# Kernel tuning notes

Hardware: AMD Instinct MI355X
Metric: run time of the kernel (lower is better)

Reference implementation:

```python
import jax, jax.numpy as jnp
import numpy as np

H = 81  # number_of_cells
EPS = 1e-5

def setup_inputs() -> dict:
    key = jax.random.key(0)
    ks = jax.random.split(key, 16)
    B, T, F = 512, 1024, 128
    s_ih = 1.0 / np.sqrt(H)
    inp = {
        'x':     jax.random.normal(ks[0], (B, 1, T, F), dtype=jnp.float32),
        'W_ih':  jax.random.uniform(ks[1], (3 * H, F), jnp.float32, -s_ih, s_ih),
        'W_hh':  jax.random.uniform(ks[2], (3 * H, H), jnp.float32, -s_ih, s_ih),
        'b_ih':  jax.random.uniform(ks[3], (3 * H,), jnp.float32, -s_ih, s_ih),
        'b_hh':  jax.random.uniform(ks[4], (3 * H,), jnp.float32, -s_ih, s_ih),
        'fc_w':  jax.random.uniform(ks[5], (8, H), jnp.float32, -s_ih, s_ih),
        'fc_b':  jax.random.uniform(ks[6], (8,), jnp.float32, -s_ih, s_ih),
        'g1':    jnp.ones((8,), jnp.float32),
        'beta1': jnp.zeros((8,), jnp.float32),
        'fc1_w': jax.random.uniform(ks[7], (4, 8), jnp.float32, -np.sqrt(1/8), np.sqrt(1/8)),
        'fc1_b': jax.random.uniform(ks[8], (4,), jnp.float32, -np.sqrt(1/8), np.sqrt(1/8)),
        'g2':    jnp.ones((4,), jnp.float32),
        'beta2': jnp.zeros((4,), jnp.float32),
        'fc2_w': jax.random.uniform(ks[9], (1, 4), jnp.float32, -0.5, 0.5),
        'fc2_b': jax.random.uniform(ks[10], (1,), jnp.float32, -0.5, 0.5),
    }
    return inp

def _batchnorm(x, g, b):
    mu = jnp.mean(x, axis=0)
    var = jnp.var(x, axis=0)  # biased, as torch uses for normalization
    return (x - mu) * jax.lax.rsqrt(var + EPS) * g + b

def _gru_last_hidden(x, W_ih, W_hh, b_ih, b_hh):
    # x: [B, T, F]; PyTorch gate order: r, z, n
    B = x.shape[0]
    xg = jnp.einsum('btf,gf->tbg', x, W_ih) + b_ih  # [T, B, 3H]
    h0 = jnp.zeros((B, H), x.dtype)

    def step(h, xg_t):
        hg = h @ W_hh.T + b_hh
        xr, xz, xn = jnp.split(xg_t, 3, axis=-1)
        hr, hz, hn = jnp.split(hg, 3, axis=-1)
        r = jax.nn.sigmoid(xr + hr)
        z = jax.nn.sigmoid(xz + hz)
        n = jnp.tanh(xn + r * hn)
        h_new = (1.0 - z) * n + z * h
        return h_new, None

    h_last, _ = jax.lax.scan(step, h0, xg)
    return h_last  # [B, H]

def reference(x, W_ih, W_hh, b_ih, b_hh, fc_w, fc_b, g1, beta1, fc1_w, fc1_b, g2, beta2, fc2_w, fc2_b):
    B = x.shape[0]
    xs = x.reshape(B, x.shape[2], x.shape[3])  # view(B, T, F)
    h = _gru_last_hidden(xs, W_ih, W_hh, b_ih, b_hh)
    out = h @ fc_w.T + fc_b            # GRU0.fc on last timestep -> [B, 8]
    out = jax.nn.silu(out)
    out = _batchnorm(out, g1, beta1)
    out = jax.nn.silu(out @ fc1_w.T + fc1_b)
    out = _batchnorm(out, g2, beta2)
    out = out @ fc2_w.T + fc2_b        # [B, 1]
    return out
```

## Files before the change

kernel.cpp:

```cpp
#include <hip/hip_runtime.h>

#define B_  512
#define T_  1024
#define F_  128
#define H_  81
#define G3  243
#define GPX 244

typedef unsigned short u16;
typedef __attribute__((ext_vector_type(8))) short bf16x8;
typedef __attribute__((ext_vector_type(4))) float f32x4;
typedef __attribute__((ext_vector_type(2))) float f32x2;

__device__ __forceinline__ float bf2f(u16 u) {
    union { unsigned int i; float f; } v; v.i = ((unsigned int)u) << 16; return v.f;
}
__device__ __forceinline__ u16 f2bf(float f) {
    union { float f; unsigned int i; } v; v.f = f;
    unsigned int i = v.i;
    return (u16)((i + 0x7fffu + ((i >> 16) & 1u)) >> 16);
}
__device__ __forceinline__ float sigmoidf_(float x) { return 1.f / (1.f + __expf(-x)); }
__device__ __forceinline__ float tanhf_(float x) {
    float e = __expf(2.f * x);
    return 1.f - 2.f / (e + 1.f);
}
__device__ __forceinline__ void barrier_nodrain() {
    asm volatile("s_waitcnt lgkmcnt(0)\n\ts_barrier" ::: "memory");
}

__global__ void wsplit_kernel(const float* __restrict__ W,
                              u16* __restrict__ hi, u16* __restrict__ lo)
{
    const int i = blockIdx.x * 256 + threadIdx.x;
    if (i < G3 * F_) {
        const float v = W[i];
        const u16 h = f2bf(v);
        hi[i] = h;
        lo[i] = f2bf(v - bf2f(h));
    }
}

__global__ __launch_bounds__(256, 2) void xg_gemm(const float* __restrict__ x,
                                                  const u16* __restrict__ Whi,
                                                  const u16* __restrict__ Wlo,
                                                  const float* __restrict__ b_ih,
                                                  float* __restrict__ xg)
{
    __shared__ __align__(16) u16 ws_hi[G3][64];
    __shared__ __align__(16) u16 ws_lo[G3][64];

    const int tid  = threadIdx.x;
    const int wave = tid >> 6, lane = tid & 63;
    const int l15  = lane & 15, q = lane >> 4;
    const int b    = blockIdx.x & 511;
    const int t0   = (blockIdx.x >> 9) << 7;

    f32x4 acc[2][16];
#pragma unroll
    for (int mt = 0; mt < 2; ++mt)
#pragma unroll
        for (int gt = 0; gt < 16; ++gt) acc[mt][gt] = (f32x4){0.f, 0.f, 0.f, 0.f};

    for (int half = 0; half < 2; ++half) {
        if (half) __syncthreads();
#pragma unroll
        for (int it = 0; it < 16; ++it) {
            const int i = it * 256 + tid;
            if (i < 2 * G3 * 8) {
                const bool lo = (i >= G3 * 8);
                const int j = lo ? (i - G3 * 8) : i;
                const int g = j >> 3, c = j & 7;
                const uint4 v = *(const uint4*)((lo ? Wlo : Whi)
                                                + (size_t)g * F_ + half * 64 + c * 8);
                *(uint4*)&((lo ? ws_lo : ws_hi)[g][((c + g) & 7) * 8]) = v;
            }
        }
        __syncthreads();

#pragma unroll
        for (int kcl = 0; kcl < 2; ++kcl) {
            bf16x8 aHi[2], aLo[2];
#pragma unroll
            for (int mt = 0; mt < 2; ++mt) {
                const float* xr = x + ((size_t)b * T_ + t0 + (wave * 2 + mt) * 16 + l15) * F_
                                  + half * 64 + kcl * 32 + q * 8;
                float xv[8];
                *(float4*)&xv[0] = *(const float4*)(xr);
                *(float4*)&xv[4] = *(const float4*)(xr + 4);
#pragma unroll
                for (int j = 0; j < 8; ++j) {
                    const u16 h = f2bf(xv[j]);
                    aHi[mt][j] = (short)h;
                    aLo[mt][j] = (short)f2bf(xv[j] - bf2f(h));
                }
            }
#pragma unroll
            for (int gt = 0; gt < 16; ++gt) {
                const int gr  = gt * 16 + l15;
                const int grc = (gr < G3) ? gr : (G3 - 1);
                const int sl  = ((kcl * 4 + q + grc) & 7) * 8;
                const bf16x8 bHi = *(const bf16x8*)&ws_hi[grc][sl];
                const bf16x8 bLo = *(const bf16x8*)&ws_lo[grc][sl];
#pragma unroll
                for (int mt = 0; mt < 2; ++mt) {
                    acc[mt][gt] = __builtin_amdgcn_mfma_f32_16x16x32_bf16(aHi[mt], bHi, acc[mt][gt], 0, 0, 0);
                    acc[mt][gt] = __builtin_amdgcn_mfma_f32_16x16x32_bf16(aHi[mt], bLo, acc[mt][gt], 0, 0, 0);
                    acc[mt][gt] = __builtin_amdgcn_mfma_f32_16x16x32_bf16(aLo[mt], bHi, acc[mt][gt], 0, 0, 0);
                }
            }
        }
    }
#pragma unroll
    for (int gt = 0; gt < 16; ++gt) {
        const int g = gt * 16 + l15;
        if (g < G3) {
            const float bias = b_ih[g];
#pragma unroll
            for (int mt = 0; mt < 2; ++mt) {
                const int trow = t0 + (wave * 2 + mt) * 16 + q * 4;
#pragma unroll
                for (int c = 0; c < 4; ++c)
                    xg[((size_t)b * T_ + trow + c) * GPX + g] = acc[mt][gt][c] + bias;
            }
        }
    }
}

__global__ __launch_bounds__(256, 2) void gru_kernel(const float* __restrict__ xg,
                                                     const float* __restrict__ W_hh,
                                                     const float* __restrict__ b_hh,
                                                     float* __restrict__ h_out)
{
    __shared__ __align__(16) float h_s[88];
    __shared__ float part0[244];
    __shared__ float part1[244];
    __shared__ float part2[244];
    __shared__ float xn_s[84];

    const int tid = threadIdx.x, b = blockIdx.x;
    const bool act = tid < G3;
    const int p   = (tid >= 162) ? 2 : ((tid >= 81) ? 1 : 0);
    const int j   = act ? (tid - p * 81) : 0;
    const int k0  = p * 28;

    f32x2 w2[3][14];
#pragma unroll
    for (int i = 0; i < 3; ++i) {
        const float* wr = W_hh + (size_t)(j + 81 * i) * H_ + k0;
#pragma unroll
        for (int c = 0; c < 14; ++c) {
            const float e0 = (act && (k0 + 2 * c)     < H_) ? wr[2 * c]     : 0.f;
            const float e1 = (act && (k0 + 2 * c + 1) < H_) ? wr[2 * c + 1] : 0.f;
            w2[i][c] = (f32x2){e0, e1};
        }
    }
#pragma unroll
    for (int i = 0; i < 3; ++i)
#pragma unroll
        for (int c = 0; c < 14; ++c)
            asm volatile("" : "+v"(w2[i][c]));

    const bool gth = tid < H_;
    const float br = gth ? b_hh[tid]          : 0.f;
    const float bz = gth ? b_hh[H_ + tid]     : 0.f;
    const float bn = gth ? b_hh[2 * H_ + tid] : 0.f;
    float hreg = 0.f;

    if (tid < 88) h_s[tid] = 0.f;
    __syncthreads();

    float* const pp = (p == 0) ? part0 : ((p == 1) ? part1 : part2);

    const float* xp = xg + (size_t)b * T_ * GPX + (act ? tid : 0);
    float xf[4];
#pragma unroll
    for (int u = 0; u < 4; ++u) xf[u] = xp[(size_t)u * GPX];

    for (int t4 = 0; t4 < T_; t4 += 4) {
#pragma unroll
        for (int u = 0; u < 4; ++u) {
            const float xv = xf[u];
            f32x2 aA[3], aB[3];
#pragma unroll
            for (int i = 0; i < 3; ++i) { aA[i] = (f32x2){0.f, 0.f}; aB[i] = (f32x2){0.f, 0.f}; }
#pragma unroll
            for (int c = 0; c < 7; ++c) {
                const float4 h4 = ((const float4*)h_s)[p * 7 + c];
                const f32x2 hlo = {h4.x, h4.y}, hhi = {h4.z, h4.w};
#pragma unroll
                for (int i = 0; i < 3; ++i) {
                    aA[i] = __builtin_elementwise_fma(w2[i][2 * c],     hlo, aA[i]);
                    aB[i] = __builtin_elementwise_fma(w2[i][2 * c + 1], hhi, aB[i]);
                }
            }
            const f32x2 t0v = aA[0] + aB[0];
            const f32x2 t1v = aA[1] + aB[1];
            const f32x2 t2v = aA[2] + aB[2];
            float s0 = t0v.x + t0v.y;
            float s1 = t1v.x + t1v.y;
            float s2 = t2v.x + t2v.y;
            s0 += (p == 0) ? xv : 0.f;
            s1 += (p == 1) ? xv : 0.f;
            if (act) {
                if (p == 2) xn_s[j] = xv;
                pp[j]       = s0;
                pp[j + 81]  = s1;
                pp[j + 162] = s2;
            }
            barrier_nodrain();
            if (gth) {
                const float prer = part0[tid]       + part1[tid]       + part2[tid]       + br;
                const float prez = part0[tid + 81]  + part1[tid + 81]  + part2[tid + 81]  + bz;
                const float hn   = part0[tid + 162] + part1[tid + 162] + part2[tid + 162] + bn;
                const float rr = sigmoidf_(prer);
                const float zz = sigmoidf_(prez);
                const float nn = tanhf_(fmaf(rr, hn, xn_s[tid]));
                hreg = nn + zz * (hreg - nn);
                h_s[tid] = hreg;
            }
            barrier_nodrain();
            const int tn = (t4 + u + 4 < T_) ? (t4 + u + 4) : (T_ - 1);
            xf[u] = xp[(size_t)tn * GPX];
        }
    }

    if (gth) h_out[(size_t)b * H_ + tid] = hreg;
}

__device__ __forceinline__ float block_sum(float v, float* red, int tid) {
#pragma unroll
    for (int off = 32; off; off >>= 1) v += __shfl_down(v, off, 64);
    const int wid = tid >> 6;
    if ((tid & 63) == 0) red[wid] = v;
    __syncthreads();
    if (tid == 0) {
        float s = 0.f;
#pragma unroll
        for (int i = 0; i < 8; ++i) s += red[i];
        red[8] = s;
    }
    __syncthreads();
    const float s = red[8];
    __syncthreads();
    return s;
}

__global__ __launch_bounds__(512) void head_kernel(const float* __restrict__ h_out,
                                                   const float* __restrict__ fc_w,
                                                   const float* __restrict__ fc_b,
                                                   const float* __restrict__ g1,
                                                   const float* __restrict__ beta1,
                                                   const float* __restrict__ fc1_w,
                                                   const float* __restrict__ fc1_b,
                                                   const float* __restrict__ g2,
                                                   const float* __restrict__ beta2,
                                                   const float* __restrict__ fc2_w,
                                                   const float* __restrict__ fc2_b,
                                                   float* __restrict__ out)
{
    __shared__ float red[9];
    const int tid = threadIdx.x;
    const float inv = 1.f / 512.f;

    float hv[H_];
    const float* hp = h_out + (size_t)tid * H_;
#pragma unroll
    for (int c = 0; c < H_; ++c) hv[c] = hp[c];

    float o[8];
#pragma unroll
    for (int j = 0; j < 8; ++j) {
        float s = fc_b[j];
        for (int c = 0; c < H_; ++c) s += hv[c] * fc_w[j * H_ + c];
        o[j] = s * sigmoidf_(s);
    }
#pragma unroll
    for (int j = 0; j < 8; ++j) {
        const float mu = block_sum(o[j], red, tid) * inv;
        const float m2 = block_sum(o[j] * o[j], red, tid) * inv;
        o[j] = (o[j] - mu) * rsqrtf(m2 - mu * mu + 1e-5f) * g1[j] + beta1[j];
    }
    float p[4];
#pragma unroll
    for (int i = 0; i < 4; ++i) {
        float s = fc1_b[i];
#pragma unroll
        for (int j = 0; j < 8; ++j) s += o[j] * fc1_w[i * 8 + j];
        p[i] = s * sigmoidf_(s);
    }
#pragma unroll
    for (int i = 0; i < 4; ++i) {
        const float mu = block_sum(p[i], red, tid) * inv;
        const float m2 = block_sum(p[i] * p[i], red, tid) * inv;
        p[i] = (p[i] - mu) * rsqrtf(m2 - mu * mu + 1e-5f) * g2[i] + beta2[i];
    }
    float res = fc2_b[0];
#pragma unroll
    for (int i = 0; i < 4; ++i) res += p[i] * fc2_w[i];
    out[tid] = res;
}

extern "C" void kernel_launch(void* const* d_in, const int* in_sizes, int n_in,
                              void* d_out, int out_size, void* d_ws, size_t ws_size,
                              hipStream_t stream)
{
    const float* x     = (const float*)d_in[0];
    const float* W_ih  = (const float*)d_in[1];
    const float* W_hh  = (const float*)d_in[2];
    const float* b_ih  = (const float*)d_in[3];
    const float* b_hh  = (const float*)d_in[4];

    float* xg    = (float*)d_ws;
    float* h_out = xg + (size_t)B_ * T_ * GPX;
    u16*   Whi   = (u16*)(h_out + B_ * H_);
    u16*   Wlo   = Whi + G3 * F_;

    wsplit_kernel<<<dim3((G3 * F_ + 255) / 256), dim3(256), 0, stream>>>(W_ih, Whi, Wlo);
    xg_gemm<<<dim3(512 * 8), dim3(256), 0, stream>>>(x, Whi, Wlo, b_ih, xg);
    gru_kernel<<<dim3(B_), dim3(256), 0, stream>>>(xg, W_hh, b_hh, h_out);
    head_kernel<<<dim3(1), dim3(512), 0, stream>>>(h_out,
        (const float*)d_in[5], (const float*)d_in[6], (const float*)d_in[7],
        (const float*)d_in[8], (const float*)d_in[9], (const float*)d_in[10],
        (const float*)d_in[11], (const float*)d_in[12], (const float*)d_in[13],
        (const float*)d_in[14], (float*)d_out);
}
```

Before: 1.150 ms.

## Process two batch rows per GRU block and use fast reciprocal in activations

Each GRU workgroup now advances two batch sequences at once, reusing the register-resident W_hh slice for both. The grid halves to 256 blocks, so the per-step barriers and the gate-update phase are shared between two sequences, and the gate math uses threads 0-80 and 128-208. Sigmoid and tanh now use the hardware reciprocal instead of division. The cost is twice the FMA work and accumulator registers per thread and only 256 blocks, which underfills the 256 CUs at one block each and makes each block's serial chain longer.

```diff
diff --git a/kernel.cpp b/kernel.cpp
--- a/kernel.cpp
+++ b/kernel.cpp
@@ -20,10 +20,10 @@
     unsigned int i = v.i;
     return (u16)((i + 0x7fffu + ((i >> 16) & 1u)) >> 16);
 }
-__device__ __forceinline__ float sigmoidf_(float x) { return 1.f / (1.f + __expf(-x)); }
+__device__ __forceinline__ float rcp_(float x) { return __builtin_amdgcn_rcpf(x); }
+__device__ __forceinline__ float sigmoidf_(float x) { return rcp_(1.f + __expf(-x)); }
 __device__ __forceinline__ float tanhf_(float x) {
-    float e = __expf(2.f * x);
-    return 1.f - 2.f / (e + 1.f);
+    return fmaf(-2.f, rcp_(__expf(2.f * x) + 1.f), 1.f);
 }
 __device__ __forceinline__ void barrier_nodrain() {
     asm volatile("s_waitcnt lgkmcnt(0)\n\ts_barrier" ::: "memory");
@@ -127,18 +127,17 @@
     }
 }
 
-__global__ __launch_bounds__(256, 2) void gru_kernel(const float* __restrict__ xg,
+__global__ __launch_bounds__(256, 1) void gru_kernel(const float* __restrict__ xg,
                                                      const float* __restrict__ W_hh,
                                                      const float* __restrict__ b_hh,
                                                      float* __restrict__ h_out)
 {
-    __shared__ __align__(16) float h_s[88];
-    __shared__ float part0[244];
-    __shared__ float part1[244];
-    __shared__ float part2[244];
-    __shared__ float xn_s[84];
-
-    const int tid = threadIdx.x, b = blockIdx.x;
+    __shared__ __align__(16) float h_s[2][88];
+    __shared__ float part[2][3][244];
+    __shared__ float xn_s[2][84];
+
+    const int tid = threadIdx.x;
+    const int b0 = blockIdx.x * 2, b1 = b0 + 1;
     const bool act = tid < G3;
     const int p   = (tid >= 162) ? 2 : ((tid >= 81) ? 1 : 0);
     const int j   = act ? (tid - p * 81) : 0;
@@ -161,71 +160,86 @@
         for (int c = 0; c < 14; ++c)
             asm volatile("" : "+v"(w2[i][c]));
 
-    const bool gth = tid < H_;
-    const float br = gth ? b_hh[tid]          : 0.f;
-    const float bz = gth ? b_hh[H_ + tid]     : 0.f;
-    const float bn = gth ? b_hh[2 * H_ + tid] : 0.f;
+    const int gq = (tid < H_) ? 0 : ((tid >= 128 && tid < 128 + H_) ? 1 : -1);
+    const int gi = (gq == 1) ? (tid - 128) : tid;
+    const float br = (gq >= 0) ? b_hh[gi]          : 0.f;
+    const float bz = (gq >= 0) ? b_hh[H_ + gi]     : 0.f;
+    const float bn = (gq >= 0) ? b_hh[2 * H_ + gi] : 0.f;
     float hreg = 0.f;
 
-    if (tid < 88) h_s[tid] = 0.f;
+    if (tid < 176) ((float*)h_s)[tid] = 0.f;
     __syncthreads();
 
-    float* const pp = (p == 0) ? part0 : ((p == 1) ? part1 : part2);
-
-    const float* xp = xg + (size_t)b * T_ * GPX + (act ? tid : 0);
-    float xf[4];
-#pragma unroll
-    for (int u = 0; u < 4; ++u) xf[u] = xp[(size_t)u * GPX];
+    const float* xp0 = xg + (size_t)b0 * T_ * GPX + (act ? tid : 0);
+    const float* xp1 = xg + (size_t)b1 * T_ * GPX + (act ? tid : 0);
+    float xf0[4], xf1[4];
+#pragma unroll
+    for (int u = 0; u < 4; ++u) {
+        xf0[u] = xp0[(size_t)u * GPX];
+        xf1[u] = xp1[(size_t)u * GPX];
+    }
 
     for (int t4 = 0; t4 < T_; t4 += 4) {
 #pragma unroll
         for (int u = 0; u < 4; ++u) {
-            const float xv = xf[u];
-            f32x2 aA[3], aB[3];
-#pragma unroll
-            for (int i = 0; i < 3; ++i) { aA[i] = (f32x2){0.f, 0.f}; aB[i] = (f32x2){0.f, 0.f}; }
+            const float xv0 = xf0[u], xv1 = xf1[u];
+            f32x2 aA0[3], aB0[3], aA1[3], aB1[3];
+#pragma unroll
+            for (int i = 0; i < 3; ++i) {
+                aA0[i] = (f32x2){0.f, 0.f}; aB0[i] = (f32x2){0.f, 0.f};
+                aA1[i] = (f32x2){0.f, 0.f}; aB1[i] = (f32x2){0.f, 0.f};
+            }
 #pragma unroll
             for (int c = 0; c < 7; ++c) {
-                const float4 h4 = ((const float4*)h_s)[p * 7 + c];
-                const f32x2 hlo = {h4.x, h4.y}, hhi = {h4.z, h4.w};
+                const float4 h40 = ((const float4*)h_s[0])[p * 7 + c];
+                const float4 h41 = ((const float4*)h_s[1])[p * 7 + c];
+                const f32x2 lo0 = {h40.x, h40.y}, hi0 = {h40.z, h40.w};
+                const f32x2 lo1 = {h41.x, h41.y}, hi1 = {h41.z, h41.w};
 #pragma unroll
                 for (int i = 0; i < 3; ++i) {
-                    aA[i] = __builtin_elementwise_fma(w2[i][2 * c],     hlo, aA[i]);
-                    aB[i] = __builtin_elementwise_fma(w2[i][2 * c + 1], hhi, aB[i]);
+                    aA0[i] = __builtin_elementwise_fma(w2[i][2 * c],     lo0, aA0[i]);
+                    aB0[i] = __builtin_elementwise_fma(w2[i][2 * c + 1], hi0, aB0[i]);
+                    aA1[i] = __builtin_elementwise_fma(w2[i][2 * c],     lo1, aA1[i]);
+                    aB1[i] = __builtin_elementwise_fma(w2[i][2 * c + 1], hi1, aB1[i]);
                 }
             }
-            const f32x2 t0v = aA[0] + aB[0];
-            const f32x2 t1v = aA[1] + aB[1];
-            const f32x2 t2v = aA[2] + aB[2];
-            float s0 = t0v.x + t0v.y;
-            float s1 = t1v.x + t1v.y;
-            float s2 = t2v.x + t2v.y;
-            s0 += (p == 0) ? xv : 0.f;
-            s1 += (p == 1) ? xv : 0.f;
+            const f32x2 t00 = aA0[0] + aB0[0], t01 = aA0[1] + aB0[1], t02 = aA0[2] + aB0[2];
+            const f32x2 t10 = aA1[0] + aB1[0], t11 = aA1[1] + aB1[1], t12 = aA1[2] + aB1[2];
+            float s00 = t00.x + t00.y, s01 = t01.x + t01.y, s02 = t02.x + t02.y;
+            float s10 = t10.x + t10.y, s11 = t11.x + t11.y, s12 = t12.x + t12.y;
+            s00 += (p == 0) ? xv0 : 0.f;
+            s01 += (p == 1) ? xv0 : 0.f;
+            s10 += (p == 0) ? xv1 : 0.f;
+            s11 += (p == 1) ? xv1 : 0.f;
             if (act) {
-                if (p == 2) xn_s[j] = xv;
-                pp[j]       = s0;
-                pp[j + 81]  = s1;
-                pp[j + 162] = s2;
+                if (p == 2) { xn_s[0][j] = xv0; xn_s[1][j] = xv1; }
+                part[0][p][j]       = s00;
+                part[0][p][j + 81]  = s01;
+                part[0][p][j + 162] = s02;
+                part[1][p][j]       = s10;
+                part[1][p][j + 81]  = s11;
+                part[1][p][j + 162] = s12;
             }
             barrier_nodrain();
-            if (gth) {
-                const float prer = part0[tid]       + part1[tid]       + part2[tid]       + br;
-                const float prez = part0[tid + 81]  + part1[tid + 81]  + part2[tid + 81]  + bz;
-                const float hn   = part0[tid + 162] + part1[tid + 162] + part2[tid + 162] + bn;
+            if (gq >= 0) {
+                const float prer = part[gq][0][gi]       + part[gq][1][gi]       + part[gq][2][gi]       + br;
+                const float prez = part[gq][0][gi + 81]  + part[gq][1][gi + 81]  + part[gq][2][gi + 81]  + bz;
+                const float hn   = part[gq][0][gi + 162] + part[gq][1][gi + 162] + part[gq][2][gi + 162] + bn;
                 const float rr = sigmoidf_(prer);
                 const float zz = sigmoidf_(prez);
-                const float nn = tanhf_(fmaf(rr, hn, xn_s[tid]));
+                const float nn = tanhf_(fmaf(rr, hn, xn_s[gq][gi]));
                 hreg = nn + zz * (hreg - nn);
-                h_s[tid] = hreg;
+                h_s[gq][gi] = hreg;
             }
             barrier_nodrain();
             const int tn = (t4 + u + 4 < T_) ? (t4 + u + 4) : (T_ - 1);
-            xf[u] = xp[(size_t)tn * GPX];
-        }
-    }
-
-    if (gth) h_out[(size_t)b * H_ + tid] = hreg;
+            xf0[u] = xp0[(size_t)tn * GPX];
+            xf1[u] = xp1[(size_t)tn * GPX];
+        }
+    }
+
+    if (gq == 0)      h_out[(size_t)b0 * H_ + gi] = hreg;
+    else if (gq == 1) h_out[(size_t)b1 * H_ + gi] = hreg;
 }
 
 __device__ __forceinline__ float block_sum(float v, float* red, int tid) {
@@ -318,7 +332,7 @@
 
     wsplit_kernel<<<dim3((G3 * F_ + 255) / 256), dim3(256), 0, stream>>>(W_ih, Whi, Wlo);
     xg_gemm<<<dim3(512 * 8), dim3(256), 0, stream>>>(x, Whi, Wlo, b_ih, xg);
-    gru_kernel<<<dim3(B_), dim3(256), 0, stream>>>(xg, W_hh, b_hh, h_out);
+    gru_kernel<<<dim3(B_ / 2), dim3(256), 0, stream>>>(xg, W_hh, b_hh, h_out);
     head_kernel<<<dim3(1), dim3(512), 0, stream>>>(h_out,
         (const float*)d_in[5], (const float*)d_in[6], (const float*)d_in[7],
         (const float*)d_in[8], (const float*)d_in[9], (const float*)d_in[10],
```

Measured after the change: 1.153 ms. No clear change (+0.3%).
